# Performance work log

Hardware: AMD Instinct MI355X
Metric: run time of the kernel (lower is better)

The kernel has to match this reference:

```python
import jax, jax.numpy as jnp
import numpy as np

DIM = 384
K = 7          # kernel_size
FINAL = 16     # final_size
DROP_P = 0.2


def setup_inputs() -> dict:
    key = jax.random.key(0)
    k1, k2, k3, k4, k5, k6 = jax.random.split(key, 6)
    hr_feats = jax.random.normal(k1, (8, DIM, 112, 112), jnp.float32)
    guidance = jnp.zeros((1,), jnp.float32)  # unused by forward
    dropout_u = jax.random.uniform(k2, (8, FINAL, FINAL, 1), jnp.float32)
    aw = jax.random.normal(k3, (DIM,), jnp.float32) / np.sqrt(DIM).astype(np.float32)
    ab = 0.01 * jax.random.normal(k4, (1,), jnp.float32)
    w = 1.0 + 0.01 * jax.random.normal(k5, (K, K), jnp.float32)
    b = 0.01 * jax.random.normal(k6, (K, K), jnp.float32)
    return {"hr_feats": hr_feats, "guidance": guidance, "dropout_u": dropout_u,
            "aw": aw, "ab": ab, "w": w, "b": b}


def _unfold_patches(x):
    # x: [b, c, h, w] -> [b, nH, nW, K*K, c], matching torch Unfold + reshape/permute
    bs, c, h, wd = x.shape
    stride = (h - K) // (FINAL - 1)
    nH = FINAL
    nW = FINAL * (wd // h)
    r = (jnp.arange(nH) * stride)[:, None] + jnp.arange(K)      # [nH, K]
    cc = (jnp.arange(nW) * stride)[:, None] + jnp.arange(K)     # [nW, K]
    # advanced indexing -> [b, c, nH, nW, K, K]
    patches = x[:, :, r[:, None, :, None], cc[None, :, None, :]]
    # (kh, kw) flattened row-major, channel last -> same ordering as torch Unfold
    return patches.transpose(0, 2, 3, 4, 5, 1).reshape(bs, nH, nW, K * K, c)


def reference(hr_feats, guidance, dropout_u, aw, ab, w, b):
    patches = _unfold_patches(hr_feats)                    # [b, H, W, P, C]
    # attention_net (eval-mode Dropout is identity): Linear(dim, 1)
    logits = jnp.einsum('bhwpc,c->bhwp', patches, aw) + ab[0]
    mask = (dropout_u > DROP_P).astype(logits.dtype)       # [b, H, W, 1]
    attn_logits = logits * mask * w.reshape(1, 1, 1, -1) + b.reshape(1, 1, 1, -1)
    attn = jax.nn.softmax(attn_logits, axis=-1)            # softmax over patches
    return jnp.einsum('bhwpc,bhwp->bchw', patches, attn)   # [b, C, H, W]
```

## Files before the change

kernel.cpp:

```cpp
#include <hip/hip_runtime.h>
#include <cmath>

#define DIM 384
#define IMG 112
#define IMG2 (IMG*IMG)
#define FINALN 16
#define PATCH 49
#define SPST 50
#define DROP_P 0.2f

__global__ __launch_bounds__(512, 4) void kFused(const float* __restrict__ hr,
                                                 const float* __restrict__ du,
                                                 const float* __restrict__ aw,
                                                 const float* __restrict__ ab,
                                                 const float* __restrict__ wmat,
                                                 const float* __restrict__ bmat,
                                                 float* __restrict__ out) {
    __shared__ float sp[DIM * SPST];
    __shared__ float s_red[8 * PATCH];

    int tid = threadIdx.x;

    int id  = blockIdx.x;
    int nid = (id & 7) * 256 + (id >> 3);
    int b = nid >> 8;
    int h = (nid >> 4) & 15;
    int w = nid & 15;

    float duv = 0.f, abv = 0.f, wv = 0.f, bv = 0.f;
    if (tid < 64) {
        if (tid < PATCH) { wv = wmat[tid]; bv = bmat[tid]; }
        duv = du[(b << 8) + (h << 4) + w];
        abv = ab[0];
    }

    int g = tid >> 3;
    int j = tid & 7;
    const float* base = hr + (size_t)b * DIM * IMG2 + (size_t)(7 * h) * IMG + 7 * w;
    const float* gp = base + (size_t)g * 6 * IMG2 + j;

    float awr[6];
    #pragma unroll
    for (int cc = 0; cc < 6; ++cc) awr[cc] = aw[g * 6 + cc];

    float part[7] = {0.f, 0.f, 0.f, 0.f, 0.f, 0.f, 0.f};
    if (j < 7) {
        float v[42];
        #pragma unroll
        for (int it = 0; it < 42; ++it) {
            const int cc = it / 7, s = it % 7;
            v[it] = gp[(size_t)cc * IMG2 + s * IMG];
        }
        float* lp = sp + g * 6 * SPST + j;
        #pragma unroll
        for (int it = 0; it < 42; ++it) {
            const int cc = it / 7, s = it % 7;
            lp[cc * SPST + s * 7] = v[it];
            part[s] = fmaf(v[it], awr[cc], part[s]);
        }
    }

    #pragma unroll
    for (int s = 0; s < 7; ++s) {
        part[s] += __shfl_xor(part[s], 8, 64);
        part[s] += __shfl_xor(part[s], 16, 64);
        part[s] += __shfl_xor(part[s], 32, 64);
    }
    int wave = tid >> 6, lane = tid & 63;
    if (lane < 7) {
        #pragma unroll
        for (int s = 0; s < 7; ++s)
            s_red[wave * PATCH + s * 7 + lane] = part[s];
    }
    __syncthreads();

    if (tid < 64) {
        float al = -1e30f;
        if (tid < PATCH) {
            float logit = abv;
            #pragma unroll
            for (int gg = 0; gg < 8; ++gg) logit += s_red[gg * PATCH + tid];
            float mask = (duv > DROP_P) ? 1.0f : 0.0f;
            al = fmaf(logit * mask, wv, bv);
        }
        float m = al;
        #pragma unroll
        for (int d = 32; d >= 1; d >>= 1) m = fmaxf(m, __shfl_xor(m, d, 64));
        float e = (tid < PATCH) ? __expf(al - m) : 0.f;
        float s = e;
        #pragma unroll
        for (int d = 32; d >= 1; d >>= 1) s += __shfl_xor(s, d, 64);
        if (tid < PATCH) s_red[tid] = e / s;
    }
    __syncthreads();

    if (tid < DIM) {
        const float* pc = sp + tid * SPST;
        float acc = 0.f;
        #pragma unroll
        for (int k = 0; k < 24; ++k) {
            float2 v2 = *reinterpret_cast<const float2*>(pc + 2 * k);
            acc = fmaf(v2.x, s_red[2 * k],     acc);
            acc = fmaf(v2.y, s_red[2 * k + 1], acc);
        }
        acc = fmaf(pc[48], s_red[48], acc);
        out[(((size_t)b * DIM + tid) * FINALN + h) * FINALN + w] = acc;
    }
}

extern "C" void kernel_launch(void* const* d_in, const int* in_sizes, int n_in,
                              void* d_out, int out_size, void* d_ws, size_t ws_size,
                              hipStream_t stream) {
    const float* hr   = (const float*)d_in[0];
    const float* du   = (const float*)d_in[2];
    const float* aw   = (const float*)d_in[3];
    const float* ab   = (const float*)d_in[4];
    const float* wmat = (const float*)d_in[5];
    const float* bmat = (const float*)d_in[6];
    float* out = (float*)d_out;

    kFused<<<2048, 512, 0, stream>>>(hr, du, aw, ab, wmat, bmat, out);
}
```

Before: 244.8 us.

## Split fused kernel into coalesced logits pass and register-only output pass

Adds a kLogits kernel that reads each channel plane with coalesced float4 loads, accumulates per-channel-group partial logits, and writes them to workspace. A second kernel, kOut, re-reads the patch values into registers, sums the partial logits, runs the softmax, and forms the weighted sum with shuffle reductions instead of a large shared-memory patch buffer. Dropping that buffer is meant to raise occupancy and cut the latency of the strided gathers. The cost is reading the input twice plus a partial-logit round trip through workspace. The old fused kernel remains as a fallback when no workspace is available.

```diff
diff --git a/kernel.cpp b/kernel.cpp
--- a/kernel.cpp
+++ b/kernel.cpp
@@ -8,6 +8,148 @@
 #define PATCH 49
 #define SPST 50
 #define DROP_P 0.2f
+#define NCG 32
+#define CPG 12
+#define PSLICE (FINALN*FINALN*PATCH)
+
+__global__ __launch_bounds__(448) void kLogits(const float* __restrict__ hr,
+                                               const float* __restrict__ aw,
+                                               float* __restrict__ part) {
+    __shared__ float sl[PSLICE];
+    int t = threadIdx.x;
+    int bidx = blockIdx.x;
+    int b  = bidx >> 5;
+    int cg = bidx & 31;
+    int c0 = cg * CPG;
+
+    const float* base = hr + (size_t)(b * DIM + c0) * IMG2;
+
+    float acc[7][4];
+    #pragma unroll
+    for (int k = 0; k < 7; ++k) { acc[k][0]=acc[k][1]=acc[k][2]=acc[k][3]=0.f; }
+
+    for (int c = 0; c < CPG; ++c) {
+        float av = aw[c0 + c];
+        const float* pc = base + (size_t)c * IMG2;
+        #pragma unroll
+        for (int k = 0; k < 7; ++k) {
+            int id = t + 448 * k;
+            float4 v = *reinterpret_cast<const float4*>(pc + 4 * id);
+            acc[k][0] = fmaf(v.x, av, acc[k][0]);
+            acc[k][1] = fmaf(v.y, av, acc[k][1]);
+            acc[k][2] = fmaf(v.z, av, acc[k][2]);
+            acc[k][3] = fmaf(v.w, av, acc[k][3]);
+        }
+    }
+    #pragma unroll
+    for (int k = 0; k < 7; ++k) {
+        int id = t + 448 * k;
+        int r = id / 28;
+        int colq = id - r * 28;
+        int h = r / 7, i = r - h * 7;
+        #pragma unroll
+        for (int e = 0; e < 4; ++e) {
+            int col = colq * 4 + e;
+            int w = col / 7, j = col - w * 7;
+            sl[(h * FINALN + w) * PATCH + i * 7 + j] = acc[k][e];
+        }
+    }
+    __syncthreads();
+    float* dst = part + (size_t)bidx * PSLICE;
+    #pragma unroll
+    for (int k = 0; k < 7; ++k) {
+        int id = t + 448 * k;
+        *reinterpret_cast<float4*>(dst + 4 * id) =
+            *reinterpret_cast<const float4*>(sl + 4 * id);
+    }
+}
+
+__global__ __launch_bounds__(512, 4) void kOut(const float* __restrict__ hr,
+                                               const float* __restrict__ part,
+                                               const float* __restrict__ du,
+                                               const float* __restrict__ ab,
+                                               const float* __restrict__ wmat,
+                                               const float* __restrict__ bmat,
+                                               float* __restrict__ out) {
+    __shared__ float s_red[8 * PATCH];
+    int tid = threadIdx.x;
+    int id  = blockIdx.x;
+    int nid = (id & 7) * 256 + (id >> 3);
+    int b = nid >> 8, h = (nid >> 4) & 15, w = nid & 15;
+    int hw = (h << 4) + w;
+
+    int g = tid >> 3, j = tid & 7;
+    const float* gp = hr + (size_t)b * DIM * IMG2 + (size_t)(7 * h) * IMG + 7 * w
+                    + (size_t)g * 6 * IMG2 + j;
+    float v[42];
+    if (j < 7) {
+        #pragma unroll
+        for (int it = 0; it < 42; ++it) {
+            const int cc = it / 7, s = it % 7;
+            v[it] = gp[(size_t)cc * IMG2 + s * IMG];
+        }
+    }
+
+    float duv = 0.f, abv = 0.f, wv = 0.f, bv = 0.f;
+    if (tid < 64) {
+        if (tid < PATCH) { wv = wmat[tid]; bv = bmat[tid]; }
+        duv = du[(b << 8) + hw];
+        abv = ab[0];
+    }
+
+    if (tid < 8 * PATCH) {
+        int g2 = tid / PATCH, p = tid - g2 * PATCH;
+        const float* pp = part + ((size_t)(b * NCG + g2 * 4)) * PSLICE
+                        + (size_t)hw * PATCH + p;
+        s_red[tid] = pp[0] + pp[PSLICE] + pp[2 * (size_t)PSLICE]
+                   + pp[3 * (size_t)PSLICE];
+    }
+    __syncthreads();
+
+    if (tid < 64) {
+        float al = -1e30f;
+        if (tid < PATCH) {
+            float logit = abv;
+            #pragma unroll
+            for (int gg = 0; gg < 8; ++gg) logit += s_red[gg * PATCH + tid];
+            float mask = (duv > DROP_P) ? 1.0f : 0.0f;
+            al = fmaf(logit * mask, wv, bv);
+        }
+        float m = al;
+        #pragma unroll
+        for (int d = 32; d >= 1; d >>= 1) m = fmaxf(m, __shfl_xor(m, d, 64));
+        float e = (tid < PATCH) ? __expf(al - m) : 0.f;
+        float s = e;
+        #pragma unroll
+        for (int d = 32; d >= 1; d >>= 1) s += __shfl_xor(s, d, 64);
+        if (tid < PATCH) s_red[tid] = e / s;
+    }
+    __syncthreads();
+
+    float att[7];
+    int js = (j < 7) ? j : 0;
+    #pragma unroll
+    for (int s = 0; s < 7; ++s) att[s] = s_red[s * 7 + js];
+    float oacc[6] = {0.f, 0.f, 0.f, 0.f, 0.f, 0.f};
+    if (j < 7) {
+        #pragma unroll
+        for (int cc = 0; cc < 6; ++cc)
+            #pragma unroll
+            for (int s = 0; s < 7; ++s)
+                oacc[cc] = fmaf(v[cc * 7 + s], att[s], oacc[cc]);
+    }
+    #pragma unroll
+    for (int cc = 0; cc < 6; ++cc) {
+        oacc[cc] += __shfl_xor(oacc[cc], 1, 64);
+        oacc[cc] += __shfl_xor(oacc[cc], 2, 64);
+        oacc[cc] += __shfl_xor(oacc[cc], 4, 64);
+    }
+    if (j == 0) {
+        size_t ob = ((size_t)b * DIM + g * 6) * 256 + hw;
+        #pragma unroll
+        for (int cc = 0; cc < 6; ++cc) out[ob + (size_t)cc * 256] = oacc[cc];
+    }
+}
 
 __global__ __launch_bounds__(512, 4) void kFused(const float* __restrict__ hr,
                                                  const float* __restrict__ du,
@@ -18,31 +160,22 @@
                                                  float* __restrict__ out) {
     __shared__ float sp[DIM * SPST];
     __shared__ float s_red[8 * PATCH];
-
     int tid = threadIdx.x;
-
     int id  = blockIdx.x;
     int nid = (id & 7) * 256 + (id >> 3);
-    int b = nid >> 8;
-    int h = (nid >> 4) & 15;
-    int w = nid & 15;
-
+    int b = nid >> 8, h = (nid >> 4) & 15, w = nid & 15;
     float duv = 0.f, abv = 0.f, wv = 0.f, bv = 0.f;
     if (tid < 64) {
         if (tid < PATCH) { wv = wmat[tid]; bv = bmat[tid]; }
         duv = du[(b << 8) + (h << 4) + w];
         abv = ab[0];
     }
-
-    int g = tid >> 3;
-    int j = tid & 7;
+    int g = tid >> 3, j = tid & 7;
     const float* base = hr + (size_t)b * DIM * IMG2 + (size_t)(7 * h) * IMG + 7 * w;
     const float* gp = base + (size_t)g * 6 * IMG2 + j;
-
     float awr[6];
     #pragma unroll
     for (int cc = 0; cc < 6; ++cc) awr[cc] = aw[g * 6 + cc];
-
     float part[7] = {0.f, 0.f, 0.f, 0.f, 0.f, 0.f, 0.f};
     if (j < 7) {
         float v[42];
@@ -59,7 +192,6 @@
             part[s] = fmaf(v[it], awr[cc], part[s]);
         }
     }
-
     #pragma unroll
     for (int s = 0; s < 7; ++s) {
         part[s] += __shfl_xor(part[s], 8, 64);
@@ -69,11 +201,9 @@
     int wave = tid >> 6, lane = tid & 63;
     if (lane < 7) {
         #pragma unroll
-        for (int s = 0; s < 7; ++s)
-            s_red[wave * PATCH + s * 7 + lane] = part[s];
-    }
-    __syncthreads();
-
+        for (int s = 0; s < 7; ++s) s_red[wave * PATCH + s * 7 + lane] = part[s];
+    }
+    __syncthreads();
     if (tid < 64) {
         float al = -1e30f;
         if (tid < PATCH) {
@@ -93,14 +223,13 @@
         if (tid < PATCH) s_red[tid] = e / s;
     }
     __syncthreads();
-
     if (tid < DIM) {
         const float* pc = sp + tid * SPST;
         float acc = 0.f;
         #pragma unroll
         for (int k = 0; k < 24; ++k) {
             float2 v2 = *reinterpret_cast<const float2*>(pc + 2 * k);
-            acc = fmaf(v2.x, s_red[2 * k],     acc);
+            acc = fmaf(v2.x, s_red[2 * k], acc);
             acc = fmaf(v2.y, s_red[2 * k + 1], acc);
         }
         acc = fmaf(pc[48], s_red[48], acc);
@@ -119,5 +248,12 @@
     const float* bmat = (const float*)d_in[6];
     float* out = (float*)d_out;
 
-    kFused<<<2048, 512, 0, stream>>>(hr, du, aw, ab, wmat, bmat, out);
-}
+    size_t need = (size_t)8 * NCG * PSLICE * sizeof(float);
+    if (d_ws != nullptr && ws_size >= need) {
+        float* part = (float*)d_ws;
+        kLogits<<<256, 448, 0, stream>>>(hr, aw, part);
+        kOut<<<2048, 512, 0, stream>>>(hr, part, du, ab, wmat, bmat, out);
+    } else {
+        kFused<<<2048, 512, 0, stream>>>(hr, du, aw, ab, wmat, bmat, out);
+    }
+}
```

After: 267.8 us. +9.4%, slower.
